# Kernel optimization log

Measured on AMD Instinct MI355X. Metric: run time of the kernel, lower is better.

Reference implementation:

```python
import jax, jax.numpy as jnp
import numpy as np

B, N, CIN, COUT, K = 8, 2048, 128, 256, 16


def setup_inputs() -> dict:
    key = jax.random.key(0)
    ks = jax.random.split(key, 8)
    xyz = jax.random.normal(ks[0], (B, 3, N), jnp.float32)
    features = jax.random.normal(ks[1], (B, CIN, N), jnp.float32)
    # 1x1 conv1d weights == dense (out, in) matrices
    W_spec = jax.random.normal(ks[2], (COUT, CIN), jnp.float32) * 0.05
    b_spec = jnp.zeros((COUT,), jnp.float32)
    bn_gamma = jnp.ones((COUT,), jnp.float32)
    bn_beta = jnp.zeros((COUT,), jnp.float32)
    bn_mean = jnp.zeros((COUT,), jnp.float32)
    bn_var = jnp.ones((COUT,), jnp.float32)
    W_low = jax.random.normal(ks[3], (COUT // 2, COUT), jnp.float32) * 0.05
    b_low = jnp.zeros((COUT // 2,), jnp.float32)
    W_high = jax.random.normal(ks[4], (COUT // 2, COUT), jnp.float32) * 0.05
    b_high = jnp.zeros((COUT // 2,), jnp.float32)
    return dict(xyz=xyz, features=features, W_spec=W_spec, b_spec=b_spec,
                bn_gamma=bn_gamma, bn_beta=bn_beta, bn_mean=bn_mean, bn_var=bn_var,
                W_low=W_low, b_low=b_low, W_high=W_high, b_high=b_high)


def reference(xyz, features, W_spec, b_spec, bn_gamma, bn_beta, bn_mean, bn_var,
              W_low, b_low, W_high, b_high):
    b, _, n = xyz.shape
    # --- graph Laplacian ---
    x = jnp.transpose(xyz, (0, 2, 1))                      # (B, N, 3)
    sq = jnp.sum(x * x, axis=-1)                           # (B, N)
    dist = sq[:, :, None] + sq[:, None, :] - 2.0 * jnp.einsum('bnd,bmd->bnm', x, x)
    _, idx = jax.lax.top_k(-dist, K)                       # (B, N, K) nearest neighbors
    b_idx = jnp.arange(b)[:, None, None]
    p_idx = jnp.arange(n)[None, :, None]
    A = jnp.zeros((b, n, n), jnp.float32).at[b_idx, p_idx, idx].set(1.0)
    A = (A + jnp.transpose(A, (0, 2, 1))) * 0.5
    D = jnp.sum(A, axis=-1)                                # (B, N)
    d = jax.lax.rsqrt(D + 1e-6)                            # D^{-1/2}
    L = jnp.eye(n, dtype=jnp.float32)[None] - d[:, :, None] * A * d[:, None, :]
    # --- spectral transform: (L @ feat^T)^T ---
    spec = jnp.einsum('bnm,bcm->bcn', L, features)         # (B, CIN, N)
    # 1x1 conv + BN (eval) + exact GELU
    spec = jnp.einsum('oc,bcn->bon', W_spec, spec) + b_spec[None, :, None]
    spec = (spec - bn_mean[None, :, None]) * jax.lax.rsqrt(bn_var + 1e-5)[None, :, None]
    spec = spec * bn_gamma[None, :, None] + bn_beta[None, :, None]
    spec = jax.nn.gelu(spec, approximate=False)
    low = jnp.einsum('oc,bcn->bon', W_low, spec) + b_low[None, :, None]
    high = jnp.einsum('oc,bcn->bon', W_high, spec) + b_high[None, :, None]
    return jnp.concatenate([low, high], axis=1)            # (B, COUT, N)
```

## Files before the change

kernel.cpp:

```cpp
#include <hip/hip_runtime.h>
#include <hip/hip_bf16.h>
#include <math.h>

#define BB   8
#define NN   2048
#define BN   (BB * NN)
#define CINC 128
#define COU  256
#define KNNK 16
#define REVCAP 64
#define QG   32

typedef __bf16 bf16x8 __attribute__((ext_vector_type(8)));
typedef float  f32x4  __attribute__((ext_vector_type(4)));

#define FMED3(dst, a, bb_, c) asm("v_med3_f32 %0, %1, %2, %3" : "=v"(dst) : "v"(a), "v"(bb_), "v"(c))

#define INF32 (__builtin_inff())

#define TOP_DECL \
    float t0=INF32,t1=INF32,t2=INF32,t3=INF32,t4=INF32,t5=INF32,t6=INF32,t7=INF32, \
          t8=INF32,t9=INF32,t10=INF32,t11=INF32,t12=INF32,t13=INF32,t14=INF32,t15=INF32;

#define TOP_INSERT(u) {                     \
    FMED3(t15, t14, t15, (u));              \
    FMED3(t14, t13, t14, (u));              \
    FMED3(t13, t12, t13, (u));              \
    FMED3(t12, t11, t12, (u));              \
    FMED3(t11, t10, t11, (u));              \
    FMED3(t10, t9,  t10, (u));              \
    FMED3(t9,  t8,  t9,  (u));              \
    FMED3(t8,  t7,  t8,  (u));              \
    FMED3(t7,  t6,  t7,  (u));              \
    FMED3(t6,  t5,  t6,  (u));              \
    FMED3(t5,  t4,  t5,  (u));              \
    FMED3(t4,  t3,  t4,  (u));              \
    FMED3(t3,  t2,  t3,  (u));              \
    FMED3(t2,  t1,  t2,  (u));              \
    FMED3(t1,  t0,  t1,  (u));              \
    t0 = fminf(t0, (u));                    \
}

#define TOP8_INSERT(u) {                    \
    FMED3(t7,  t6,  t7,  (u));              \
    FMED3(t6,  t5,  t6,  (u));              \
    FMED3(t5,  t4,  t5,  (u));              \
    FMED3(t4,  t3,  t4,  (u));              \
    FMED3(t3,  t2,  t3,  (u));              \
    FMED3(t2,  t1,  t2,  (u));              \
    FMED3(t1,  t0,  t1,  (u));              \
    t0 = fminf(t0, (u));                    \
}

static __device__ __forceinline__ float dist_f(float qx, float qy, float qz,
                                               float qsq, float4 c) {
    float dot = fmaf(qz, c.z, fmaf(qy, c.y, __fmul_rn(qx, c.x)));
    return __fsub_rn(__fadd_rn(qsq, c.w), __fmul_rn(2.0f, dot));
}

__global__ __launch_bounds__(256) void setup_kernel(const float* __restrict__ feat,
                                                    __bf16* __restrict__ fTB,
                                                    const float* __restrict__ Wspec,
                                                    const float* __restrict__ Wlow,
                                                    const float* __restrict__ Whigh,
                                                    const float* __restrict__ blow,
                                                    const float* __restrict__ bhigh,
                                                    __bf16* __restrict__ WspecB,
                                                    __bf16* __restrict__ WcB,
                                                    float* __restrict__ bc,
                                                    int* __restrict__ rcnt) {
    __shared__ float t[32][33];
    int bid = blockIdx.x;
    int tx = threadIdx.x, ty = threadIdx.y;
    if (bid < 2048) {
        int b  = bid >> 8;
        int r  = bid & 255;
        int n0 = (r & 63) * 32;
        int c0 = (r >> 6) * 32;
#pragma unroll
        for (int i = 0; i < 4; i++)
            t[ty + i * 8][tx] = feat[((size_t)b * CINC + c0 + ty + i * 8) * NN + n0 + tx];
        __syncthreads();
#pragma unroll
        for (int i = 0; i < 4; i++)
            fTB[((size_t)b * NN + n0 + ty + i * 8) * CINC + c0 + tx] = (__bf16)t[tx][ty + i * 8];
    } else {
        int r = bid - 2048;
        int i = r * 256 + ty * 32 + tx;
        if (i < COU * CINC) WspecB[i] = (__bf16)Wspec[i];
        if (i < 128 * COU) {
            WcB[i] = (__bf16)Wlow[i];
            WcB[128 * COU + i] = (__bf16)Whigh[i];
        }
        if (i < 128) { bc[i] = blow[i]; bc[128 + i] = bhigh[i]; }
        rcnt[r * 128 + (ty * 32 + tx) % 128] = 0;
    }
}

__global__ __launch_bounds__(1024, 8) void knn_fused_kernel(const float* __restrict__ xyz,
                                                            int* __restrict__ knn_idx,
                                                            int* __restrict__ revcnt,
                                                            int* __restrict__ rev) {
    __shared__ float4 cand[NN];
    __shared__ float mbuf[8][KNNK][QG];
    __shared__ float Tq[QG];
    __shared__ int cntless[QG];
    __shared__ int tiecnt[QG];
    __shared__ unsigned short tieidx[16][QG];
    __shared__ unsigned short sel[KNNK][QG];

    int b = blockIdx.y;
    int lane = threadIdx.x & 63;
    int w = threadIdx.x >> 6;
    int q32 = lane & 31;
    int qh = lane >> 5;
    int q = blockIdx.x * QG + q32;
    int bq = b * NN + q;

    const float* xb = xyz + (size_t)b * 3 * NN;
#pragma unroll
    for (int t0i = 0; t0i < 2; t0i++) {
        int t = threadIdx.x + t0i * 1024;
        float x = xb[t], y = xb[NN + t], z = xb[2 * NN + t];
        float sq = __fadd_rn(__fadd_rn(__fmul_rn(x, x), __fmul_rn(y, y)), __fmul_rn(z, z));
        cand[t] = make_float4(x, y, z, sq);
    }
    if (threadIdx.x < QG) { cntless[threadIdx.x] = 0; tiecnt[threadIdx.x] = 0; }
    __syncthreads();

    float qx = xb[q], qy = xb[NN + q], qz = xb[2 * NN + q];
    float qsq = __fadd_rn(__fadd_rn(__fmul_rn(qx, qx), __fmul_rn(qy, qy)), __fmul_rn(qz, qz));

    int segbase = w * 128 + qh * 64;

    TOP_DECL
#pragma unroll
    for (int i = 0; i < 64; i += 4) {
        float4 c0 = cand[segbase + i + 0];
        float4 c1 = cand[segbase + i + 1];
        float4 c2 = cand[segbase + i + 2];
        float4 c3 = cand[segbase + i + 3];
        float d0 = dist_f(qx, qy, qz, qsq, c0);
        float d1 = dist_f(qx, qy, qz, qsq, c1);
        float d2 = dist_f(qx, qy, qz, qsq, c2);
        float d3 = dist_f(qx, qy, qz, qsq, c3);
        TOP8_INSERT(d0)
        TOP8_INSERT(d1)
        TOP8_INSERT(d2)
        TOP8_INSERT(d3)
    }

    {
        float s0 = __shfl_xor(t0, 32), s1 = __shfl_xor(t1, 32);
        float s2 = __shfl_xor(t2, 32), s3 = __shfl_xor(t3, 32);
        float s4 = __shfl_xor(t4, 32), s5 = __shfl_xor(t5, 32);
        float s6 = __shfl_xor(t6, 32), s7 = __shfl_xor(t7, 32);
        TOP_INSERT(s0) TOP_INSERT(s1) TOP_INSERT(s2) TOP_INSERT(s3)
        TOP_INSERT(s4) TOP_INSERT(s5) TOP_INSERT(s6) TOP_INSERT(s7)
    }

    for (int s = 8; s >= 1; s >>= 1) {
        if (w >= s && w < 2 * s && lane < 32) {
            int j = w - s;
            mbuf[j][0][q32] = t0;   mbuf[j][1][q32] = t1;
            mbuf[j][2][q32] = t2;   mbuf[j][3][q32] = t3;
            mbuf[j][4][q32] = t4;   mbuf[j][5][q32] = t5;
            mbuf[j][6][q32] = t6;   mbuf[j][7][q32] = t7;
            mbuf[j][8][q32] = t8;   mbuf[j][9][q32] = t9;
            mbuf[j][10][q32] = t10; mbuf[j][11][q32] = t11;
            mbuf[j][12][q32] = t12; mbuf[j][13][q32] = t13;
            mbuf[j][14][q32] = t14; mbuf[j][15][q32] = t15;
        }
        __syncthreads();
        if (w < s) {
#pragma unroll
            for (int k = 0; k < KNNK; k++) {
                float u = mbuf[w][k][q32];
                TOP_INSERT(u)
            }
        }
        __syncthreads();
    }
    if (w == 0 && lane < 32) Tq[q32] = t15;
    __syncthreads();

    {
        float T = Tq[q32];
#pragma unroll
        for (int i = 0; i < 64; i++) {
            float4 c = cand[segbase + i];
            float du = dist_f(qx, qy, qz, qsq, c);
            if (du < T) {
                int slot = atomicAdd(&cntless[q32], 1);
                if (slot < 16) sel[slot][q32] = (unsigned short)(segbase + i);
            } else if (du == T) {
                int t = atomicAdd(&tiecnt[q32], 1);
                if (t < 16) tieidx[t][q32] = (unsigned short)(segbase + i);
            }
        }
    }
    __syncthreads();

    if (threadIdx.x < QG) {
        int cl = cntless[threadIdx.x];
        if (cl >= 16) {
            TOP_DECL
            for (int i = 0; i < NN; i++) {
                float du = dist_f(qx, qy, qz, qsq, cand[i]);
                TOP_INSERT(du)
            }
            float Tt = t15;
            int fp = 0;
            for (int i = 0; i < NN && fp < KNNK; i++) {
                float du = dist_f(qx, qy, qz, qsq, cand[i]);
                if (du < Tt) sel[fp++][threadIdx.x] = (unsigned short)i;
            }
            for (int i = 0; i < NN && fp < KNNK; i++) {
                float du = dist_f(qx, qy, qz, qsq, cand[i]);
                if (du == Tt) sel[fp++][threadIdx.x] = (unsigned short)i;
            }
        } else {
            float T = Tq[threadIdx.x];
            int need = KNNK - cl;
            int tc = tiecnt[threadIdx.x];
            if (need > 0) {
                if (tc <= 16) {
                    for (int r = 0; r < need; r++) {
                        int best = 0x7fffffff, bj = 0;
                        for (int j = 0; j < tc; j++) {
                            int v = tieidx[j][threadIdx.x];
                            if (v < best) { best = v; bj = j; }
                        }
                        tieidx[bj][threadIdx.x] = 0xFFFF;
                        sel[cl + r][threadIdx.x] = (unsigned short)best;
                    }
                } else {
                    int em = 0;
                    for (int i = 0; i < NN && em < need; i++) {
                        float du = dist_f(qx, qy, qz, qsq, cand[i]);
                        if (du == T) { sel[cl + em][threadIdx.x] = (unsigned short)i; em++; }
                    }
                }
            }
        }
    }
    __syncthreads();

    if (lane < 32) {
        int x = (int)sel[w][q32];
        knn_idx[(size_t)bq * KNNK + w] = x;
        int pos = atomicAdd(&revcnt[b * NN + x], 1);
        if (pos < REVCAP) rev[((size_t)(b * NN + x)) * REVCAP + pos] = q;
    }
}

__global__ __launch_bounds__(128) void spec_kernel(const __bf16* __restrict__ fTB,
                                                   const int* __restrict__ knn_idx,
                                                   const int* __restrict__ revcnt,
                                                   const int* __restrict__ rev,
                                                   __bf16* __restrict__ specB) {
    __shared__ int ml[KNNK + REVCAP];
    __shared__ float wl[KNNK + REVCAP];
    __shared__ int s_cnt;
    __shared__ float s_dn;

    int bn = blockIdx.x;
    int b = bn >> 11;
    int tid = threadIdx.x;

    if (tid == 0) {
        int c = revcnt[bn];
        s_cnt = c < REVCAP ? c : REVCAP;
        float D = 0.5f * (float)(KNNK + c);
        s_dn = 1.0f / sqrtf(D + 1e-6f);
    }
    __syncthreads();
    int cnt = s_cnt;
    if (tid < KNNK) ml[tid] = knn_idx[(size_t)bn * KNNK + tid];
    if (tid < cnt) ml[KNNK + tid] = rev[(size_t)bn * REVCAP + tid];
    __syncthreads();
    int total = KNNK + cnt;
    if (tid < total) {
        int m = ml[tid];
        float D = 0.5f * (float)(KNNK + revcnt[b * NN + m]);
        wl[tid] = 0.5f * (1.0f / sqrtf(D + 1e-6f));
    }
    __syncthreads();

    const __bf16* base = fTB + (size_t)b * NN * CINC + tid;
    float acc0 = 0.0f, acc1 = 0.0f, acc2 = 0.0f, acc3 = 0.0f;
    int j = 0;
    for (; j + 4 <= total; j += 4) {
        float f0v = (float)base[(size_t)ml[j + 0] * CINC];
        float f1v = (float)base[(size_t)ml[j + 1] * CINC];
        float f2v = (float)base[(size_t)ml[j + 2] * CINC];
        float f3v = (float)base[(size_t)ml[j + 3] * CINC];
        acc0 = fmaf(wl[j + 0], f0v, acc0);
        acc1 = fmaf(wl[j + 1], f1v, acc1);
        acc2 = fmaf(wl[j + 2], f2v, acc2);
        acc3 = fmaf(wl[j + 3], f3v, acc3);
    }
    for (; j < total; j++)
        acc0 = fmaf(wl[j], (float)base[(size_t)ml[j] * CINC], acc0);
    float acc = (acc0 + acc1) + (acc2 + acc3);

    float f0 = (float)base[(size_t)(bn & (NN - 1)) * CINC];
    specB[(size_t)bn * CINC + tid] = (__bf16)(f0 - s_dn * acc);
}

__global__ __launch_bounds__(256) void gemm12_fused(const __bf16* __restrict__ specB,
                                                    const __bf16* __restrict__ WspecB,
                                                    const float* __restrict__ bspec,
                                                    const float* __restrict__ gamma,
                                                    const float* __restrict__ beta,
                                                    const float* __restrict__ mean,
                                                    const float* __restrict__ var,
                                                    const __bf16* __restrict__ WcB,
                                                    const float* __restrict__ bc,
                                                    float* __restrict__ out) {
    __shared__ __bf16 g1s[64][COU + 8];
    int b  = blockIdx.y;
    int n0 = blockIdx.x * 64;
    int w = threadIdx.x >> 6, lane = threadIdx.x & 63;
    int lr = lane & 15, lk = (lane >> 4) * 8;
    int rb = (lane >> 4) * 4;

    {
        int o0 = w * 64;
        f32x4 acc[4][4] = {};
        const __bf16* As = specB + ((size_t)b * NN + n0 + lr) * CINC + lk;
        const __bf16* Bs = WspecB + (size_t)(o0 + lr) * CINC + lk;
#pragma unroll
        for (int kk = 0; kk < CINC; kk += 32) {
            bf16x8 a[4], bb[4];
#pragma unroll
            for (int m = 0; m < 4; m++)
                a[m] = *(const bf16x8*)(As + (size_t)(m * 16) * CINC + kk);
#pragma unroll
            for (int n = 0; n < 4; n++)
                bb[n] = *(const bf16x8*)(Bs + (size_t)(n * 16) * CINC + kk);
#pragma unroll
            for (int m = 0; m < 4; m++)
#pragma unroll
                for (int n = 0; n < 4; n++)
                    acc[m][n] = __builtin_amdgcn_mfma_f32_16x16x32_bf16(a[m], bb[n], acc[m][n], 0, 0, 0);
        }
#pragma unroll
        for (int n = 0; n < 4; n++) {
            int o = o0 + n * 16 + lr;
            float sc = 1.0f / sqrtf(var[o] + 1e-5f);
            float ga = gamma[o], be = beta[o], mu = mean[o], bs = bspec[o];
#pragma unroll
            for (int m = 0; m < 4; m++) {
#pragma unroll
                for (int j = 0; j < 4; j++) {
                    int nrow = m * 16 + rb + j;
                    float y = acc[m][n][j] + bs;
                    y = (y - mu) * sc;
                    y = y * ga + be;
                    float g = 0.5f * y * (1.0f + erff(y * 0.70710678118654752440f));
                    g1s[nrow][o] = (__bf16)g;
                }
            }
        }
    }
    __syncthreads();

    {
        int o0 = w * 64;
        f32x4 acc[4][4] = {};
        const __bf16* As = WcB + (size_t)(o0 + lr) * COU + lk;
#pragma unroll
        for (int kk = 0; kk < COU; kk += 32) {
            bf16x8 a[4], bb[4];
#pragma unroll
            for (int m = 0; m < 4; m++)
                a[m] = *(const bf16x8*)(As + (size_t)(m * 16) * COU + kk);
#pragma unroll
            for (int n = 0; n < 4; n++)
                bb[n] = *(const bf16x8*)(&g1s[n * 16 + lr][kk + lk]);
#pragma unroll
            for (int m = 0; m < 4; m++)
#pragma unroll
                for (int n = 0; n < 4; n++)
                    acc[m][n] = __builtin_amdgcn_mfma_f32_16x16x32_bf16(a[m], bb[n], acc[m][n], 0, 0, 0);
        }
#pragma unroll
        for (int m = 0; m < 4; m++) {
#pragma unroll
            for (int j = 0; j < 4; j++) {
                int o = o0 + m * 16 + rb + j;
                float bias = bc[o];
#pragma unroll
                for (int n = 0; n < 4; n++) {
                    int ncol = n0 + n * 16 + lr;
                    out[((size_t)b * COU + o) * NN + ncol] = acc[m][n][j] + bias;
                }
            }
        }
    }
}

extern "C" void kernel_launch(void* const* d_in, const int* in_sizes, int n_in,
                              void* d_out, int out_size, void* d_ws, size_t ws_size,
                              hipStream_t stream) {
    const float* xyz      = (const float*)d_in[0];
    const float* features = (const float*)d_in[1];
    const float* W_spec   = (const float*)d_in[2];
    const float* b_spec   = (const float*)d_in[3];
    const float* bn_gamma = (const float*)d_in[4];
    const float* bn_beta  = (const float*)d_in[5];
    const float* bn_mean  = (const float*)d_in[6];
    const float* bn_var   = (const float*)d_in[7];
    const float* W_low    = (const float*)d_in[8];
    const float* b_low    = (const float*)d_in[9];
    const float* W_high   = (const float*)d_in[10];
    const float* b_high   = (const float*)d_in[11];
    float* out = (float*)d_out;

    char* ws = (char*)d_ws;
    size_t off = 0;
    __bf16* fTB   = (__bf16*)(ws + off); off += (size_t)BB * NN * CINC * 2;
    __bf16* specB = (__bf16*)(ws + off); off += (size_t)BB * NN * CINC * 2;
    int*    idx   = (int*)(ws + off);    off += (size_t)BB * NN * KNNK * 4;
    int*    rcnt  = (int*)(ws + off);    off += (size_t)BB * NN * 4;
    int*    rev   = (int*)(ws + off);    off += (size_t)BB * NN * REVCAP * 4;
    __bf16* WspecB= (__bf16*)(ws + off); off += (size_t)COU * CINC * 2;
    __bf16* WcB   = (__bf16*)(ws + off); off += (size_t)COU * COU * 2;
    float*  bc    = (float*)(ws + off);  off += (size_t)COU * 4;

    setup_kernel<<<dim3(2048 + 128), dim3(32, 8), 0, stream>>>(
        features, fTB, W_spec, W_low, W_high, b_low, b_high, WspecB, WcB, bc, rcnt);
    knn_fused_kernel<<<dim3(NN / QG, BB), dim3(1024), 0, stream>>>(xyz, idx, rcnt, rev);
    spec_kernel<<<dim3(BB * NN), dim3(128), 0, stream>>>(fTB, idx, rcnt, rev, specB);
    gemm12_fused<<<dim3(NN / 64, BB), dim3(256), 0, stream>>>(
        specB, WspecB, b_spec, bn_gamma, bn_beta, bn_mean, bn_var, WcB, bc, out);
}
```

Measured before the change: 89.19 us.

## Shrink KNN block to 16 queries with 512 threads and intra-wave shuffle merge

Each KNN block now handles 16 queries with 8 waves instead of 32 queries with 16 waves. Each wave covers 4 candidate segments per query, merged with two shuffle stages (xor 16 and xor 32) before a shorter 3-level shared-memory tree. This doubles the block count for more scheduling flexibility and cuts cross-wave barrier rounds. In exchange, every block reloads the full 2048-point candidate set into LDS twice as often, and the final index write-out is remapped to the new thread layout.

```diff
diff --git a/kernel.cpp b/kernel.cpp
--- a/kernel.cpp
+++ b/kernel.cpp
@@ -9,7 +9,7 @@
 #define COU  256
 #define KNNK 16
 #define REVCAP 64
-#define QG   32
+#define QG   16
 
 typedef __bf16 bf16x8 __attribute__((ext_vector_type(8)));
 typedef float  f32x4  __attribute__((ext_vector_type(4)));
@@ -97,12 +97,12 @@
     }
 }
 
-__global__ __launch_bounds__(1024, 8) void knn_fused_kernel(const float* __restrict__ xyz,
-                                                            int* __restrict__ knn_idx,
-                                                            int* __restrict__ revcnt,
-                                                            int* __restrict__ rev) {
+__global__ __launch_bounds__(512, 8) void knn_fused_kernel(const float* __restrict__ xyz,
+                                                           int* __restrict__ knn_idx,
+                                                           int* __restrict__ revcnt,
+                                                           int* __restrict__ rev) {
     __shared__ float4 cand[NN];
-    __shared__ float mbuf[8][KNNK][QG];
+    __shared__ float mbuf[4][KNNK][QG];
     __shared__ float Tq[QG];
     __shared__ int cntless[QG];
     __shared__ int tiecnt[QG];
@@ -112,15 +112,15 @@
     int b = blockIdx.y;
     int lane = threadIdx.x & 63;
     int w = threadIdx.x >> 6;
-    int q32 = lane & 31;
-    int qh = lane >> 5;
-    int q = blockIdx.x * QG + q32;
+    int q16 = lane & 15;
+    int qh = lane >> 4;
+    int q = blockIdx.x * QG + q16;
     int bq = b * NN + q;
 
     const float* xb = xyz + (size_t)b * 3 * NN;
 #pragma unroll
-    for (int t0i = 0; t0i < 2; t0i++) {
-        int t = threadIdx.x + t0i * 1024;
+    for (int t0i = 0; t0i < 4; t0i++) {
+        int t = threadIdx.x + t0i * 512;
         float x = xb[t], y = xb[NN + t], z = xb[2 * NN + t];
         float sq = __fadd_rn(__fadd_rn(__fmul_rn(x, x), __fmul_rn(y, y)), __fmul_rn(z, z));
         cand[t] = make_float4(x, y, z, sq);
@@ -131,7 +131,7 @@
     float qx = xb[q], qy = xb[NN + q], qz = xb[2 * NN + q];
     float qsq = __fadd_rn(__fadd_rn(__fmul_rn(qx, qx), __fmul_rn(qy, qy)), __fmul_rn(qz, qz));
 
-    int segbase = w * 128 + qh * 64;
+    int segbase = w * 256 + qh * 64;
 
     TOP_DECL
 #pragma unroll
@@ -151,51 +151,65 @@
     }
 
     {
-        float s0 = __shfl_xor(t0, 32), s1 = __shfl_xor(t1, 32);
-        float s2 = __shfl_xor(t2, 32), s3 = __shfl_xor(t3, 32);
-        float s4 = __shfl_xor(t4, 32), s5 = __shfl_xor(t5, 32);
-        float s6 = __shfl_xor(t6, 32), s7 = __shfl_xor(t7, 32);
+        float s0 = __shfl_xor(t0, 16), s1 = __shfl_xor(t1, 16);
+        float s2 = __shfl_xor(t2, 16), s3 = __shfl_xor(t3, 16);
+        float s4 = __shfl_xor(t4, 16), s5 = __shfl_xor(t5, 16);
+        float s6 = __shfl_xor(t6, 16), s7 = __shfl_xor(t7, 16);
         TOP_INSERT(s0) TOP_INSERT(s1) TOP_INSERT(s2) TOP_INSERT(s3)
         TOP_INSERT(s4) TOP_INSERT(s5) TOP_INSERT(s6) TOP_INSERT(s7)
     }
-
-    for (int s = 8; s >= 1; s >>= 1) {
-        if (w >= s && w < 2 * s && lane < 32) {
+    {
+        float s0 = __shfl_xor(t0, 32),  s1 = __shfl_xor(t1, 32);
+        float s2 = __shfl_xor(t2, 32),  s3 = __shfl_xor(t3, 32);
+        float s4 = __shfl_xor(t4, 32),  s5 = __shfl_xor(t5, 32);
+        float s6 = __shfl_xor(t6, 32),  s7 = __shfl_xor(t7, 32);
+        float s8 = __shfl_xor(t8, 32),  s9 = __shfl_xor(t9, 32);
+        float s10 = __shfl_xor(t10, 32), s11 = __shfl_xor(t11, 32);
+        float s12 = __shfl_xor(t12, 32), s13 = __shfl_xor(t13, 32);
+        float s14 = __shfl_xor(t14, 32), s15 = __shfl_xor(t15, 32);
+        TOP_INSERT(s0)  TOP_INSERT(s1)  TOP_INSERT(s2)  TOP_INSERT(s3)
+        TOP_INSERT(s4)  TOP_INSERT(s5)  TOP_INSERT(s6)  TOP_INSERT(s7)
+        TOP_INSERT(s8)  TOP_INSERT(s9)  TOP_INSERT(s10) TOP_INSERT(s11)
+        TOP_INSERT(s12) TOP_INSERT(s13) TOP_INSERT(s14) TOP_INSERT(s15)
+    }
+
+    for (int s = 4; s >= 1; s >>= 1) {
+        if (w >= s && w < 2 * s && lane < QG) {
             int j = w - s;
-            mbuf[j][0][q32] = t0;   mbuf[j][1][q32] = t1;
-            mbuf[j][2][q32] = t2;   mbuf[j][3][q32] = t3;
-            mbuf[j][4][q32] = t4;   mbuf[j][5][q32] = t5;
-            mbuf[j][6][q32] = t6;   mbuf[j][7][q32] = t7;
-            mbuf[j][8][q32] = t8;   mbuf[j][9][q32] = t9;
-            mbuf[j][10][q32] = t10; mbuf[j][11][q32] = t11;
-            mbuf[j][12][q32] = t12; mbuf[j][13][q32] = t13;
-            mbuf[j][14][q32] = t14; mbuf[j][15][q32] = t15;
+            mbuf[j][0][q16] = t0;   mbuf[j][1][q16] = t1;
+            mbuf[j][2][q16] = t2;   mbuf[j][3][q16] = t3;
+            mbuf[j][4][q16] = t4;   mbuf[j][5][q16] = t5;
+            mbuf[j][6][q16] = t6;   mbuf[j][7][q16] = t7;
+            mbuf[j][8][q16] = t8;   mbuf[j][9][q16] = t9;
+            mbuf[j][10][q16] = t10; mbuf[j][11][q16] = t11;
+            mbuf[j][12][q16] = t12; mbuf[j][13][q16] = t13;
+            mbuf[j][14][q16] = t14; mbuf[j][15][q16] = t15;
         }
         __syncthreads();
         if (w < s) {
 #pragma unroll
             for (int k = 0; k < KNNK; k++) {
-                float u = mbuf[w][k][q32];
+                float u = mbuf[w][k][q16];
                 TOP_INSERT(u)
             }
         }
         __syncthreads();
     }
-    if (w == 0 && lane < 32) Tq[q32] = t15;
+    if (w == 0 && lane < QG) Tq[q16] = t15;
     __syncthreads();
 
     {
-        float T = Tq[q32];
+        float T = Tq[q16];
 #pragma unroll
         for (int i = 0; i < 64; i++) {
             float4 c = cand[segbase + i];
             float du = dist_f(qx, qy, qz, qsq, c);
             if (du < T) {
-                int slot = atomicAdd(&cntless[q32], 1);
-                if (slot < 16) sel[slot][q32] = (unsigned short)(segbase + i);
+                int slot = atomicAdd(&cntless[q16], 1);
+                if (slot < 16) sel[slot][q16] = (unsigned short)(segbase + i);
             } else if (du == T) {
-                int t = atomicAdd(&tiecnt[q32], 1);
-                if (t < 16) tieidx[t][q32] = (unsigned short)(segbase + i);
+                int t = atomicAdd(&tiecnt[q16], 1);
+                if (t < 16) tieidx[t][q16] = (unsigned short)(segbase + i);
             }
         }
     }
@@ -246,11 +260,14 @@
     }
     __syncthreads();
 
-    if (lane < 32) {
-        int x = (int)sel[w][q32];
-        knn_idx[(size_t)bq * KNNK + w] = x;
+    if (threadIdx.x < 256) {
+        int k = threadIdx.x >> 4;
+        int qq = threadIdx.x & 15;
+        int x = (int)sel[k][qq];
+        int bq2 = b * NN + blockIdx.x * QG + qq;
+        knn_idx[(size_t)bq2 * KNNK + k] = x;
         int pos = atomicAdd(&revcnt[b * NN + x], 1);
-        if (pos < REVCAP) rev[((size_t)(b * NN + x)) * REVCAP + pos] = q;
+        if (pos < REVCAP) rev[((size_t)(b * NN + x)) * REVCAP + pos] = blockIdx.x * QG + qq;
     }
 }
 
@@ -431,7 +448,7 @@
 
     setup_kernel<<<dim3(2048 + 128), dim3(32, 8), 0, stream>>>(
         features, fTB, W_spec, W_low, W_high, b_low, b_high, WspecB, WcB, bc, rcnt);
-    knn_fused_kernel<<<dim3(NN / QG, BB), dim3(1024), 0, stream>>>(xyz, idx, rcnt, rev);
+    knn_fused_kernel<<<dim3(NN / QG, BB), dim3(512), 0, stream>>>(xyz, idx, rcnt, rev);
     spec_kernel<<<dim3(BB * NN), dim3(128), 0, stream>>>(fTB, idx, rcnt, rev, specB);
     gemm12_fused<<<dim3(NN / 64, BB), dim3(256), 0, stream>>>(
         specB, WspecB, b_spec, bn_gamma, bn_beta, bn_mean, bn_var, WcB, bc, out);
```

New measurement: 91.66 us. 2.8% more time.
